# Kernel optimization log

Hardware: AMD Instinct MI355X
Metric: run time of the kernel (lower is better)

Reference implementation:

```python
import jax, jax.numpy as jnp
import numpy as np
import math

ENC_MAX = 64
DEC_MAX = 128


def _tran_mask(M):
    # faithful reconstruction of self.tran and self.mask buffers
    fs = math.log(DEC_MAX / (DEC_MAX + ENC_MAX))  # fixed_shift_p
    fe = math.log(ENC_MAX / (DEC_MAX + ENC_MAX))  # fixed_emit_p
    i = np.arange(M)[:, None]
    j = np.arange(M)[None, :]
    tran = np.where(i + j < M, (M - (i + j) - 1) * fs + fe, 0.0).astype(np.float32)
    # mask_br: -inf where i+j >= M (anti-diagonal i+j==M-1 stays 0)
    mask = np.where(i + j >= M, -np.inf, 0.0).astype(np.float32)
    return jnp.asarray(tran), jnp.asarray(mask)


def _lstm(xs, Wih, Whh, bih, bhh):
    # xs: [L, in]; torch LSTM gate order i,f,g,o; batch=1 handled as unbatched
    H = Whh.shape[1]
    def step(carry, xt):
        h, c = carry
        g = Wih @ xt + bih + Whh @ h + bhh  # [4H]
        i, f, gg, o = jnp.split(g, 4)
        c = jax.nn.sigmoid(f) * c + jax.nn.sigmoid(i) * jnp.tanh(gg)
        h = jax.nn.sigmoid(o) * jnp.tanh(c)
        return (h, c), h
    _, hs = jax.lax.scan(step, (jnp.zeros((H,), xs.dtype), jnp.zeros((H,), xs.dtype)), xs)
    return hs  # [L, H]


def setup_inputs() -> dict:
    key = jax.random.key(0)
    ks = jax.random.split(key, 16)
    V, E, H, K, T = 32000, 100, 512, ENC_MAX, DEC_MAX
    def p(k, shape, scale):
        return jax.random.normal(k, shape, dtype=jnp.float32) * scale
    return {
        "x": jax.random.randint(ks[0], (1, K), 0, V),
        "y": jax.random.randint(ks[1], (1, T), 0, V),
        "emb": p(ks[2], (V, E), 0.1),
        "enc_Wih": p(ks[3], (4 * H, E), 1.0 / np.sqrt(E)),
        "enc_Whh": p(ks[4], (4 * H, H), 1.0 / np.sqrt(H)),
        "enc_bih": jnp.zeros((4 * H,), jnp.float32),
        "enc_bhh": jnp.zeros((4 * H,), jnp.float32),
        "dec_Wih": p(ks[5], (4 * H, E), 1.0 / np.sqrt(E)),
        "dec_Whh": p(ks[6], (4 * H, H), 1.0 / np.sqrt(H)),
        "dec_bih": jnp.zeros((4 * H,), jnp.float32),
        "dec_bhh": jnp.zeros((4 * H,), jnp.float32),
        "Weh": p(ks[7], (E, 2 * H), 1.0 / np.sqrt(2 * H)),  # emit_hidden
        "beh": jnp.zeros((E,), jnp.float32),
        "Wem": p(ks[8], (V, E), 1.0 / np.sqrt(E)),  # emit
        "bem": jnp.zeros((V,), jnp.float32),
    }


def reference(x, y, emb, enc_Wih, enc_Whh, enc_bih, enc_bhh,
              dec_Wih, dec_Whh, dec_bih, dec_bhh, Weh, beh, Wem, bem):
    K = x.shape[1]
    T = y.shape[1]
    x_emb = emb[x[0]]            # [K, E]
    y_emb = emb[y[0]]            # [T, E]
    Eenc = _lstm(x_emb, enc_Wih, enc_Whh, enc_bih, enc_bhh)  # [K, H]
    D = _lstm(y_emb, dec_Wih, dec_Whh, dec_bih, dec_bhh)     # [T, H]

    tran, mask = _tran_mask(ENC_MAX)
    tranm = tran[ENC_MAX - K:, :K] + mask[ENC_MAX - K:, :K]  # [K, K]

    # emissions for all steps at once (joint = cat(E, D_{t-1}) -> relu -> emit -> log_softmax -> gather word_t)
    H = Eenc.shape[1]
    We_E, We_D = Weh[:, :H], Weh[:, H:]
    hpre = jax.nn.relu(Eenc @ We_E.T + (D[:T - 1] @ We_D.T)[:, None, :] + beh)  # [T-1, K, E]
    logits = jnp.einsum('tke,ve->tkv', hpre, Wem) + bem                          # [T-1, K, V]
    words = y[0, 1:]                                                             # [T-1]
    gathered = jnp.take_along_axis(logits, words[:, None, None], axis=2)[..., 0]  # [T-1, K]
    emission = gathered - jax.scipy.special.logsumexp(logits, axis=2)             # [T-1, K]

    def step(pre_alpha, em_t):
        scores = pre_alpha[:, None] + tranm            # [K(i), K(j)]
        mx = jnp.max(scores, axis=0)                   # [K]
        ind = jnp.argmax(scores, axis=0).astype(jnp.int32)
        mx = jnp.flip(mx)                              # self.flip
        ind = jnp.flip(ind)
        new = mx + em_t
        return new, ind

    pre_alpha, inds = jax.lax.scan(step, jnp.zeros((K,), jnp.float32), emission)
    indices = jnp.concatenate([jnp.zeros((1, K), jnp.int32), inds], axis=0)  # [T, K]

    val = pre_alpha[K - 1]  # align_last

    def bstep(ind, idx_row):
        nind = idx_row[ind]
        return nind, nind
    _, alignments = jax.lax.scan(bstep, jnp.int32(K - 1), indices, reverse=True)  # [T]
    return alignments, val
```

## Files before the change

kernel.cpp:

```cpp
#include <hip/hip_runtime.h>


#define K_ENC 64
#define HID   512
#define EMB   100
#define VOC   32000
#define G4    2048

typedef __attribute__((ext_vector_type(8))) short  short8;
typedef __attribute__((ext_vector_type(4))) float  f32x4;
typedef unsigned long long u64;

#define LOG2E 1.4426950408889634f
#define LN2   0.6931471805599453f

__device__ __forceinline__ unsigned short f2bf(float f) {
  union { float f; unsigned u; } x; x.f = f;
  unsigned r = x.u + 0x7FFFu + ((x.u >> 16) & 1u);
  return (unsigned short)(r >> 16);
}

__device__ __forceinline__ float fast_sigmoid(float x) {
  return __builtin_amdgcn_rcpf(1.f + __builtin_amdgcn_exp2f(-LOG2E * x));
}
__device__ __forceinline__ float fast_tanh(float x) {
  return 1.f - 2.f * __builtin_amdgcn_rcpf(1.f + __builtin_amdgcn_exp2f(2.f * LOG2E * x));
}

#define OFF_PAD   0
#define OFF_HBUF  256
#define OFF_G0E   4352
#define OFF_G0D   135424
#define OFF_EENC  395520
#define OFF_D     428288
#define OFF_EWE   493312
#define OFF_DWD   499712
#define OFF_BEM   512412
#define OFF_SUM   544412
#define OFF_EM    552540
#define OFF_WEM   560668

__global__ void kZero(float* __restrict__ ws) {
  int gid = blockIdx.x * 256 + threadIdx.x;
  if (gid < 4352) ws[gid] = 0.f;
  else if (gid < 4352 + 127 * 64) ws[OFF_SUM + gid - 4352] = 0.f;
}

__global__ __launch_bounds__(256) void kG0(const int* __restrict__ x, const int* __restrict__ y,
                    const float* __restrict__ emb,
                    const float* __restrict__ eWih, const float* __restrict__ ebih,
                    const float* __restrict__ ebhh,
                    const float* __restrict__ dWih, const float* __restrict__ dbih,
                    const float* __restrict__ dbhh,
                    float* __restrict__ ws) {
  int gid = blockIdx.x * 256 + threadIdx.x;
  const int enc_total = K_ENC * G4;
  if (gid >= enc_total + 127 * G4) return;
  bool enc = gid < enc_total;
  int loc = enc ? gid : gid - enc_total;
  int t = loc >> 11, r = loc & (G4 - 1);
  int tok = enc ? x[t] : y[t];
  const float* Wr = (enc ? eWih : dWih) + r * EMB;
  const float* er = emb + tok * EMB;
  float s = 0.f;
  #pragma unroll 4
  for (int e = 0; e < EMB; ++e) s += er[e] * Wr[e];
  s += enc ? (ebih[r] + ebhh[r]) : (dbih[r] + dbhh[r]);
  ws[(enc ? OFF_G0E : OFF_G0D) + t * G4 + r] = s;
}

__global__ __launch_bounds__(256) void kWemPrep(const float* __restrict__ Wem,
                                               const float* __restrict__ bem,
                                               float* __restrict__ ws) {
  int gid = blockIdx.x * 256 + threadIdx.x;
  int vt = gid >> 11;
  int kb = (gid >> 9) & 3;
  int L  = (gid >> 3) & 63;
  int j  = gid & 7;
  int v = vt * 16 + (L & 15);
  int k = kb * 32 + ((L >> 4) << 3) + j;
  float val = (k < EMB) ? Wem[v * EMB + k] : 0.f;
  ((unsigned short*)(ws + OFF_WEM))[gid] = f2bf(val);
  if (gid < VOC) ws[OFF_BEM + gid] = bem[gid] * LOG2E;
}

#define STEP_GUARD 16384

__global__ __launch_bounds__(512, 2) void kLstm(const float* __restrict__ eWhh,
                                                const float* __restrict__ dWhh,
                                                float* __restrict__ ws) {
  const int grp = blockIdx.x >> 5;
  const int wg  = blockIdx.x & 31;
  const float* __restrict__ Whh = grp ? dWhh : eWhh;
  const float* __restrict__ G0  = ws + (grp ? OFF_G0D : OFF_G0E);
  float* hs = ws + (grp ? OFF_D : OFF_EENC);
  float* hb = ws + OFF_HBUF + grp * 1024;
  int* cnt = (int*)ws + 32 + grp * 32;
  const int steps = grp ? 127 : K_ENC;
  const int tid = threadIdx.x;
  const int jl = tid >> 5, sub = tid & 31;
  const int j = wg * 16 + jl;
  __shared__ float h_lds[32 * 20];

  float4 w4[16];
  #pragma unroll
  for (int g = 0; g < 4; ++g)
    #pragma unroll
    for (int q = 0; q < 4; ++q)
      w4[g * 4 + q] = *(const float4*)&Whh[(g * HID + j) * HID + sub * 16 + q * 4];

  float cst = 0.f;
  for (int t = 0; t < steps; ++t) {
    float g0i = G0[t * G4 + j];
    float g0f = G0[t * G4 + HID + j];
    float g0g = G0[t * G4 + 2 * HID + j];
    float g0o = G0[t * G4 + 3 * HID + j];
    int got = 0;
    if (tid == 0 && t > 0) {
      const int target = 32 * t;
      int guard = 0;
      for (;;) {
        got = atomicOr(cnt, 0);
        if (got >= target || ++guard >= STEP_GUARD) break;
        __builtin_amdgcn_s_sleep(1);
      }
    }
    if (tid < 64) {
      const float* src = hb + (t & 1) * 512 + tid * 8;
      f32x4 a, b;
      asm volatile(
        "global_load_dwordx4 %0, %2, off sc0 sc1\n\t"
        "global_load_dwordx4 %1, %2, off offset:16 sc0 sc1\n\t"
        "s_waitcnt vmcnt(0)"
        : "=&v"(a), "=&v"(b)
        : "v"(src), "v"(got));
      #pragma unroll
      for (int i = 0; i < 8; ++i) {
        int k = tid * 8 + i;
        float v = (i < 4) ? a[i] : b[i - 4];
        h_lds[(k >> 4) * 20 + (k & 15)] = v;
      }
    }
    __syncthreads();
    float h[16];
    #pragma unroll
    for (int kk = 0; kk < 16; ++kk) h[kk] = h_lds[sub * 20 + kk];
    float p0 = 0.f, p1 = 0.f, p2 = 0.f, p3 = 0.f;
    #pragma unroll
    for (int q = 0; q < 4; ++q) {
      p0 += w4[0+q].x*h[q*4+0] + w4[0+q].y*h[q*4+1] + w4[0+q].z*h[q*4+2] + w4[0+q].w*h[q*4+3];
      p1 += w4[4+q].x*h[q*4+0] + w4[4+q].y*h[q*4+1] + w4[4+q].z*h[q*4+2] + w4[4+q].w*h[q*4+3];
      p2 += w4[8+q].x*h[q*4+0] + w4[8+q].y*h[q*4+1] + w4[8+q].z*h[q*4+2] + w4[8+q].w*h[q*4+3];
      p3 += w4[12+q].x*h[q*4+0] + w4[12+q].y*h[q*4+1] + w4[12+q].z*h[q*4+2] + w4[12+q].w*h[q*4+3];
    }
    #pragma unroll
    for (int d = 1; d <= 16; d <<= 1) {
      p0 += __shfl_xor(p0, d); p1 += __shfl_xor(p1, d);
      p2 += __shfl_xor(p2, d); p3 += __shfl_xor(p3, d);
    }
    float si = fast_sigmoid(g0i + p0);
    float sf = fast_sigmoid(g0f + p1);
    float gG = fast_tanh(g0g + p2);
    float so = fast_sigmoid(g0o + p3);
    cst = sf * cst + si * gG;
    float hn = so * fast_tanh(cst);
    if (sub == 0) {
      float* dst = hb + ((t + 1) & 1) * 512 + j;
      asm volatile(
        "global_store_dword %0, %1, off sc0 sc1\n\t"
        "s_waitcnt vmcnt(0)"
        : : "v"(dst), "v"(hn));
      hs[t * HID + j] = hn;
    }
    __syncthreads();
    if (tid == 0) atomicAdd(cnt, 1);
  }
}

__global__ __launch_bounds__(256) void kProj(const float* __restrict__ Weh,
                                             const float* __restrict__ beh,
                                             float* __restrict__ ws) {
  int bid = blockIdx.x;
  bool enc = bid < K_ENC;
  int row = enc ? bid : bid - K_ENC;
  const float* in = ws + (enc ? OFF_EENC : OFF_D) + row * HID;
  __shared__ float sin_[HID];
  int tid = threadIdx.x;
  sin_[tid] = in[tid]; sin_[tid + 256] = in[tid + 256];
  __syncthreads();
  if (tid < EMB) {
    const float* wr = Weh + tid * 1024 + (enc ? 0 : HID);
    float s = 0.f;
    #pragma unroll 4
    for (int h = 0; h < HID; ++h) s += sin_[h] * wr[h];
    if (!enc) s += beh[tid];
    ws[(enc ? OFF_EWE : OFF_DWD) + row * EMB + tid] = s * LOG2E;
  }
}

__global__ __launch_bounds__(256) void kLogits(float* __restrict__ ws) {
  const int t = blockIdx.x >> 2;
  const int chunk = blockIdx.x & 3;
  const int tid = threadIdx.x;
  const int lane = tid & 63;
  const int wv = tid >> 6;
  const int quad = lane >> 4, l15 = lane & 15;
  __shared__ __align__(16) unsigned short A[64 * 128];
  const float* EWe = ws + OFF_EWE;
  const float* DWd = ws + OFF_DWD + t * EMB;
  for (int idx = tid; idx < 64 * 128; idx += 256) {
    int m = idx >> 7, k = idx & 127;
    float hv = 0.f;
    if (k < EMB) { float s = EWe[m * EMB + k] + DWd[k]; hv = s > 0.f ? s : 0.f; }
    A[idx] = f2bf(hv);
  }
  __syncthreads();
  short8 af[4][4];
  #pragma unroll
  for (int mt = 0; mt < 4; ++mt)
    #pragma unroll
    for (int kb = 0; kb < 4; ++kb)
      af[mt][kb] = *(const short8*)&A[(mt * 16 + l15) * 128 + kb * 32 + quad * 8];
  const unsigned short* wem = (const unsigned short*)(ws + OFF_WEM);
  const float* bem_s = ws + OFF_BEM;
  float rs[4][4];
  #pragma unroll
  for (int a = 0; a < 4; ++a)
    #pragma unroll
    for (int b = 0; b < 4; ++b) rs[a][b] = 0.f;
  int vt = chunk * 500 + wv;
  short8 nb0, nb1, nb2, nb3; float nbi;
  nb0 = *(const short8*)&wem[(vt * 4 + 0) * 512 + lane * 8];
  nb1 = *(const short8*)&wem[(vt * 4 + 1) * 512 + lane * 8];
  nb2 = *(const short8*)&wem[(vt * 4 + 2) * 512 + lane * 8];
  nb3 = *(const short8*)&wem[(vt * 4 + 3) * 512 + lane * 8];
  nbi = bem_s[vt * 16 + l15];
  for (int ii = wv; ii < 500; ii += 4) {
    short8 cb0 = nb0, cb1 = nb1, cb2 = nb2, cb3 = nb3;
    float cbi = nbi;
    int nvt = vt + 4;
    if (ii + 4 < 500) {
      nb0 = *(const short8*)&wem[(nvt * 4 + 0) * 512 + lane * 8];
      nb1 = *(const short8*)&wem[(nvt * 4 + 1) * 512 + lane * 8];
      nb2 = *(const short8*)&wem[(nvt * 4 + 2) * 512 + lane * 8];
      nb3 = *(const short8*)&wem[(nvt * 4 + 3) * 512 + lane * 8];
      nbi = bem_s[nvt * 16 + l15];
    }
    f32x4 acc[4];
    #pragma unroll
    for (int mt = 0; mt < 4; ++mt) acc[mt] = (f32x4){cbi, cbi, cbi, cbi};
    #pragma unroll
    for (int mt = 0; mt < 4; ++mt) {
      acc[mt] = __builtin_amdgcn_mfma_f32_16x16x32_bf16(af[mt][0], cb0, acc[mt], 0, 0, 0);
      acc[mt] = __builtin_amdgcn_mfma_f32_16x16x32_bf16(af[mt][1], cb1, acc[mt], 0, 0, 0);
      acc[mt] = __builtin_amdgcn_mfma_f32_16x16x32_bf16(af[mt][2], cb2, acc[mt], 0, 0, 0);
      acc[mt] = __builtin_amdgcn_mfma_f32_16x16x32_bf16(af[mt][3], cb3, acc[mt], 0, 0, 0);
    }
    #pragma unroll
    for (int mt = 0; mt < 4; ++mt)
      #pragma unroll
      for (int r = 0; r < 4; ++r)
        rs[mt][r] += __builtin_amdgcn_exp2f(acc[mt][r]);
    vt = nvt;
  }
  #pragma unroll
  for (int d = 1; d < 16; d <<= 1)
    #pragma unroll
    for (int mt = 0; mt < 4; ++mt)
      #pragma unroll
      for (int r = 0; r < 4; ++r)
        rs[mt][r] += __shfl_xor(rs[mt][r], d);
  if (l15 == 0) {
    float* sum = ws + OFF_SUM + t * 64;
    #pragma unroll
    for (int mt = 0; mt < 4; ++mt)
      #pragma unroll
      for (int r = 0; r < 4; ++r)
        atomicAdd(&sum[mt * 16 + quad * 4 + r], rs[mt][r]);
  }
}

__global__ __launch_bounds__(256) void kEmission(const int* __restrict__ y,
                                                 const float* __restrict__ Wem,
                                                 float* __restrict__ ws) {
  int gid = blockIdx.x * 256 + threadIdx.x;
  if (gid >= 127 * 64) return;
  int t = gid >> 6, m = gid & 63;
  const float* ew = ws + OFF_EWE + m * EMB;
  const float* dw = ws + OFF_DWD + t * EMB;
  int wt = y[t + 1];
  const float* wr = Wem + wt * EMB;
  float s = ws[OFF_BEM + wt];
  #pragma unroll 4
  for (int e = 0; e < EMB; ++e) {
    float h = ew[e] + dw[e];
    h = h > 0.f ? h : 0.f;
    s += h * wr[e];
  }
  ws[OFF_EM + gid] = LN2 * (s - __builtin_amdgcn_logf(ws[OFF_SUM + gid]));
}

__global__ __launch_bounds__(256) void kViterbi(const float* __restrict__ ws, float* __restrict__ out) {
  __shared__ float em_lds[127 * 64];
  __shared__ int   inds[128 * 64];
  __shared__ float sval;
  const int tid = threadIdx.x;
  for (int i = tid; i < 127 * 64; i += 256) em_lds[i] = ws[OFF_EM + i];
  if (tid < 64) inds[tid] = 0;
  __syncthreads();
  if (tid < 64) {
    const int j = tid;
    const float fs = -0.4054651081081644f;
    const float fe = -1.0986122886681098f;
    float pa = 0.f;
    float emnext = em_lds[j];
    for (int t = 0; t < 127; ++t) {
      float emc = emnext;
      if (t < 126) emnext = em_lds[(t + 1) * 64 + j];
      float v = fmaf(-fs, (float)j, pa);
      int idx = j;
      #pragma unroll
      for (int d = 1; d < 64; d <<= 1) {
        float vv = __shfl_up(v, d);
        int   ii = __shfl_up(idx, d);
        bool cur = v > vv;
        v   = cur ? v : vv;
        idx = cur ? idx : ii;
      }
      pa = v + fe + fs * (float)j + emc;
      inds[(t + 1) * 64 + j] = idx;
    }
    if (j == 63) sval = pa;
  }
  __syncthreads();
  if (tid == 0) {
    int ind = 63;
    for (int t = 127; t >= 0; --t) {
      ind = inds[t * 64 + ind];
      out[t] = (float)ind;
    }
    out[128] = sval;
  }
}

extern "C" void kernel_launch(void* const* d_in, const int* in_sizes, int n_in,
                              void* d_out, int out_size, void* d_ws, size_t ws_size,
                              hipStream_t stream) {
  const int*   x    = (const int*)d_in[0];
  const int*   y    = (const int*)d_in[1];
  const float* emb  = (const float*)d_in[2];
  const float* eWih = (const float*)d_in[3];
  const float* eWhh = (const float*)d_in[4];
  const float* ebih = (const float*)d_in[5];
  const float* ebhh = (const float*)d_in[6];
  const float* dWih = (const float*)d_in[7];
  const float* dWhh = (const float*)d_in[8];
  const float* dbih = (const float*)d_in[9];
  const float* dbhh = (const float*)d_in[10];
  const float* Weh  = (const float*)d_in[11];
  const float* beh  = (const float*)d_in[12];
  const float* Wem  = (const float*)d_in[13];
  const float* bem  = (const float*)d_in[14];
  float* ws  = (float*)d_ws;
  float* out = (float*)d_out;

  hipLaunchKernelGGL(kZero,     dim3(49),    dim3(256), 0, stream, ws);
  hipLaunchKernelGGL(kG0,       dim3(1528),  dim3(256), 0, stream, x, y, emb, eWih, ebih, ebhh, dWih, dbih, dbhh, ws);
  hipLaunchKernelGGL(kWemPrep,  dim3(16000), dim3(256), 0, stream, Wem, bem, ws);
  hipLaunchKernelGGL(kLstm,     dim3(64),    dim3(512), 0, stream, eWhh, dWhh, ws);
  hipLaunchKernelGGL(kProj,     dim3(191),   dim3(256), 0, stream, Weh, beh, ws);
  hipLaunchKernelGGL(kLogits,   dim3(508),   dim3(256), 0, stream, ws);
  hipLaunchKernelGGL(kEmission, dim3(32),    dim3(256), 0, stream, y, Wem, ws);
  hipLaunchKernelGGL(kViterbi,  dim3(1),     dim3(256), 0, stream, ws, out);
}
```

Before: 593.8 us.

## Replace counter barrier with step-tagged hidden-state flags in LSTM kernel

Each hidden value is now written as a 64-bit word that packs the float with its step index. Consumers poll until the tags match the current step, which replaces the global atomic counter barrier and removes one round trip per step. The Whh weight loads also move inside the time loop, so the weights are re-read from memory every step instead of staying in registers, likely to cut register pressure. This adds per-step memory traffic and more polling threads (256 per block instead of one). The initial zero-step tag depends on how the buffer was initialized.

```diff
diff --git a/kernel.cpp b/kernel.cpp
--- a/kernel.cpp
+++ b/kernel.cpp
@@ -9,6 +9,7 @@
 
 typedef __attribute__((ext_vector_type(8))) short  short8;
 typedef __attribute__((ext_vector_type(4))) float  f32x4;
+typedef __attribute__((ext_vector_type(4))) int    i32x4;
 typedef unsigned long long u64;
 
 #define LOG2E 1.4426950408889634f
@@ -94,52 +95,40 @@
   const float* __restrict__ Whh = grp ? dWhh : eWhh;
   const float* __restrict__ G0  = ws + (grp ? OFF_G0D : OFF_G0E);
   float* hs = ws + (grp ? OFF_D : OFF_EENC);
-  float* hb = ws + OFF_HBUF + grp * 1024;
-  int* cnt = (int*)ws + 32 + grp * 32;
+  u64* hb = (u64*)(ws + OFF_HBUF) + grp * 1024;
   const int steps = grp ? 127 : K_ENC;
   const int tid = threadIdx.x;
   const int jl = tid >> 5, sub = tid & 31;
   const int j = wg * 16 + jl;
   __shared__ float h_lds[32 * 20];
 
-  float4 w4[16];
-  #pragma unroll
-  for (int g = 0; g < 4; ++g)
-    #pragma unroll
-    for (int q = 0; q < 4; ++q)
-      w4[g * 4 + q] = *(const float4*)&Whh[(g * HID + j) * HID + sub * 16 + q * 4];
-
   float cst = 0.f;
   for (int t = 0; t < steps; ++t) {
+    float4 w4[16];
+    #pragma unroll
+    for (int g = 0; g < 4; ++g)
+      #pragma unroll
+      for (int q = 0; q < 4; ++q)
+        w4[g * 4 + q] = *(const float4*)&Whh[(g * HID + j) * HID + sub * 16 + q * 4];
     float g0i = G0[t * G4 + j];
     float g0f = G0[t * G4 + HID + j];
     float g0g = G0[t * G4 + 2 * HID + j];
     float g0o = G0[t * G4 + 3 * HID + j];
-    int got = 0;
-    if (tid == 0 && t > 0) {
-      const int target = 32 * t;
+    if (tid < 256) {
+      const u64* src = hb + (t & 1) * 512 + tid * 2;
+      i32x4 v;
       int guard = 0;
       for (;;) {
-        got = atomicOr(cnt, 0);
-        if (got >= target || ++guard >= STEP_GUARD) break;
+        asm volatile("global_load_dwordx4 %0, %1, off sc0 sc1\n\t"
+                     "s_waitcnt vmcnt(0)"
+                     : "=v"(v) : "v"(src) : "memory");
+        if ((v[1] == t && v[3] == t) || ++guard >= STEP_GUARD) break;
         __builtin_amdgcn_s_sleep(1);
       }
-    }
-    if (tid < 64) {
-      const float* src = hb + (t & 1) * 512 + tid * 8;
-      f32x4 a, b;
-      asm volatile(
-        "global_load_dwordx4 %0, %2, off sc0 sc1\n\t"
-        "global_load_dwordx4 %1, %2, off offset:16 sc0 sc1\n\t"
-        "s_waitcnt vmcnt(0)"
-        : "=&v"(a), "=&v"(b)
-        : "v"(src), "v"(got));
-      #pragma unroll
-      for (int i = 0; i < 8; ++i) {
-        int k = tid * 8 + i;
-        float v = (i < 4) ? a[i] : b[i - 4];
-        h_lds[(k >> 4) * 20 + (k & 15)] = v;
-      }
+      int k0 = tid * 2, k1 = k0 + 1;
+      union { int u; float f; } c0, c1; c0.u = v[0]; c1.u = v[2];
+      h_lds[(k0 >> 4) * 20 + (k0 & 15)] = c0.f;
+      h_lds[(k1 >> 4) * 20 + (k1 & 15)] = c1.f;
     }
     __syncthreads();
     float h[16];
@@ -165,15 +154,12 @@
     cst = sf * cst + si * gG;
     float hn = so * fast_tanh(cst);
     if (sub == 0) {
-      float* dst = hb + ((t + 1) & 1) * 512 + j;
-      asm volatile(
-        "global_store_dword %0, %1, off sc0 sc1\n\t"
-        "s_waitcnt vmcnt(0)"
-        : : "v"(dst), "v"(hn));
+      union { float f; unsigned u; } hu; hu.f = hn;
+      u64 pack = ((u64)(unsigned)(t + 1) << 32) | (u64)hu.u;
+      atomicExch(&hb[((t + 1) & 1) * 512 + j], pack);
       hs[t * HID + j] = hn;
     }
     __syncthreads();
-    if (tid == 0) atomicAdd(cnt, 1);
   }
 }
 
```

After: 510.3 us. 1.16x faster.
